# Kernel optimization log

Measured on AMD Instinct MI355X. Metric: run time of the kernel, lower is better.

The kernel has to match this reference:

```python
import jax, jax.numpy as jnp
import numpy as np

DIM_X, DIM_Z, D_MODEL, N_HEADS, BATCH = 512, 256, 256, 8, 32


def sinusoidal_pe(seq_len, d_model):
    # standard sinusoidal table, rows indexed by position
    pos = np.arange(seq_len)[:, None].astype(np.float32)
    div = np.exp(np.arange(0, d_model, 2).astype(np.float32) * (-np.log(10000.0) / d_model))
    pe = np.zeros((seq_len, d_model), dtype=np.float32)
    pe[:, 0::2] = np.sin(pos * div)
    pe[:, 1::2] = np.cos(pos * div)
    return jnp.asarray(pe)


def setup_inputs() -> dict:
    key = jax.random.key(0)
    ks = jax.random.split(key, 5)
    state = jax.random.normal(ks[0], (BATCH, D_MODEL, DIM_X), dtype=jnp.float32)
    obs = jax.random.normal(ks[1], (BATCH, D_MODEL, DIM_Z), dtype=jnp.float32)
    Qp = jax.random.uniform(ks[2], (DIM_X, D_MODEL), dtype=jnp.float32)  # torch.rand init
    Wq = jax.random.normal(ks[3], (D_MODEL, D_MODEL), dtype=jnp.float32) / np.sqrt(D_MODEL)
    Wk = jax.random.normal(ks[4], (D_MODEL, D_MODEL), dtype=jnp.float32) / np.sqrt(D_MODEL)
    bq = jnp.zeros((D_MODEL,), dtype=jnp.float32)
    bk = jnp.zeros((D_MODEL,), dtype=jnp.float32)
    return {"state": state, "obs": obs, "Qp": Qp, "Wq": Wq, "bq": bq, "Wk": Wk, "bk": bk}


def reference(state, obs, Qp, Wq, bq, Wk, bk):
    bs, en, dim_x = state.shape
    dim_z = obs.shape[2]
    d_model = Qp.shape[1]
    h = N_HEADS
    hd = d_model // h
    S = dim_x + dim_z

    # mean-center over the ensemble axis
    A = state - jnp.mean(state, axis=1, keepdims=True)   # [bs, en, dim_x]
    Y = obs - jnp.mean(obs, axis=1, keepdims=True)       # [bs, en, dim_z]
    A = jnp.transpose(A, (2, 0, 1))                      # [dim_x, bs, en]
    Y = jnp.transpose(Y, (2, 0, 1))                      # [dim_z, bs, en]

    # positional encoding: batch_first=True quirk -> PE indexed along axis 1 (the bs axis)
    pe = sinusoidal_pe(bs, d_model)[None, :, :]          # [1, bs, d_model]
    query = Qp[:, None, :] + pe                          # [dim_x, bs, d_model] (broadcast of repeat)
    xy = jnp.concatenate([A, Y], axis=0) + pe            # [S, bs, d_model]

    # multi-head attention weights (V / out-proj do not affect returned quantities)
    q = (query @ Wq.T + bq).reshape(dim_x, bs, h, hd)
    k = (xy @ Wk.T + bk).reshape(S, bs, h, hd)
    scores = jnp.einsum('lbhd,sbhd->bhls', q, k) / np.sqrt(hd)  # [bs, h, dim_x, S]

    # fixed structured mask: eye(dim_x) | bottom-padded eye(dim_z)
    p1 = jnp.eye(dim_x, dtype=bool)
    p2 = jnp.concatenate([jnp.zeros((dim_x - dim_z, dim_z), dtype=bool),
                          jnp.eye(dim_z, dtype=bool)], axis=0)
    allow = jnp.concatenate([p1, p2], axis=1)            # [dim_x, S]
    scores = jnp.where(allow[None, None], scores, -jnp.inf)
    atten = jnp.mean(jax.nn.softmax(scores, axis=-1), axis=1)  # average over heads -> [bs, dim_x, S]

    # weighted merge of the ORIGINAL (uncentered) state/obs
    merge = jnp.concatenate([jnp.transpose(state, (0, 2, 1)),
                             jnp.transpose(obs, (0, 2, 1))], axis=1)  # [bs, S, en]
    new_state = jnp.einsum('bls,bse->ble', atten, merge)              # [bs, dim_x, en]
    new_state = jnp.transpose(new_state, (0, 2, 1))                   # [bs, en, dim_x]
    return new_state, atten
```

## Files before the change

### kernel.cpp

```cpp
#include <hip/hip_runtime.h>
#include <stdint.h>
#include <math.h>


#define WS_P    0
#define WS_QWT  8192
#define WS_PQ   73728
#define WS_U    81920
#define WS_V    606208

typedef float vf4 __attribute__((ext_vector_type(4)));
__device__ __forceinline__ void nt_store4(float* p, float x, float y,
                                          float z, float w) {
  vf4 v; v.x = x; v.y = y; v.z = z; v.w = w;
  __builtin_nontemporal_store(v, (vf4*)p);
}

__global__ void __launch_bounds__(256)
k_qw(const float* __restrict__ Qp, const float* __restrict__ Wq,
     float* __restrict__ ws) {
  int bid = blockIdx.x, t = threadIdx.x;
  if (bid < 64) {
    __shared__ float wq_s[32][132];
    __shared__ float qp_s[32][132];
    int d0 = (bid >> 3) << 5, j0 = (bid & 7) << 5;
    int j = t & 31, dq = t >> 5;
    float acc[4] = {0.f, 0.f, 0.f, 0.f};
    for (int ec = 0; ec < 256; ec += 128) {
      #pragma unroll
      for (int k = 0; k < 4; ++k) {
        int i = (k << 8) + t;
        int r = i >> 5, c4 = i & 31;
        *(float4*)&wq_s[r][c4 << 2] =
            *(const float4*)(Wq + (size_t)(d0 + r) * 256 + ec + (c4 << 2));
        *(float4*)&qp_s[r][c4 << 2] =
            *(const float4*)(Qp + 65536 + (size_t)(j0 + r) * 256 + ec + (c4 << 2));
      }
      __syncthreads();
      #pragma unroll 8
      for (int e4 = 0; e4 < 32; ++e4) {
        float4 q = *(const float4*)&qp_s[j][e4 << 2];
        #pragma unroll
        for (int r = 0; r < 4; ++r) {
          float4 w = *(const float4*)&wq_s[(dq << 2) + r][e4 << 2];
          acc[r] += w.x * q.x + w.y * q.y + w.z * q.z + w.w * q.w;
        }
      }
      __syncthreads();
    }
    #pragma unroll
    for (int r = 0; r < 4; ++r)
      ws[WS_QWT + (size_t)(d0 + (dq << 2) + r) * 256 + j0 + j] = acc[r];
  } else {
    __shared__ float wq_s[32][132];
    __shared__ float pe_s[32][132];
    int d0 = (bid - 64) << 5;
    int b = t & 31, dq = t >> 5;
    float acc[4] = {0.f, 0.f, 0.f, 0.f};
    for (int ec = 0; ec < 256; ec += 128) {
      #pragma unroll
      for (int k = 0; k < 4; ++k) {
        int i = (k << 8) + t;
        int r = i >> 5, c4 = i & 31;
        *(float4*)&wq_s[r][c4 << 2] =
            *(const float4*)(Wq + (size_t)(d0 + r) * 256 + ec + (c4 << 2));
      }
      {
        int b2 = t >> 3, e0 = (t & 7) << 4;
        #pragma unroll
        for (int k = 0; k < 16; ++k) {
          int e = e0 + k;
          int ge = ec + e;
          int k2 = ge & ~1;
          float div = expf((float)k2 * (-9.210340371976184f / 256.f));
          float a = (float)b2 * div;
          pe_s[b2][e] = (ge & 1) ? cosf(a) : sinf(a);
        }
      }
      __syncthreads();
      #pragma unroll 8
      for (int e4 = 0; e4 < 32; ++e4) {
        float4 p = *(const float4*)&pe_s[b][e4 << 2];
        #pragma unroll
        for (int r = 0; r < 4; ++r) {
          float4 w = *(const float4*)&wq_s[(dq << 2) + r][e4 << 2];
          acc[r] += w.x * p.x + w.y * p.y + w.z * p.z + w.w * p.w;
        }
      }
      __syncthreads();
    }
    #pragma unroll
    for (int r = 0; r < 4; ++r)
      ws[WS_PQ + b * 256 + d0 + (dq << 2) + r] = acc[r];
  }
}

__global__ void __launch_bounds__(256)
k_uv(const float* __restrict__ Wk, const float* __restrict__ bq,
     float* __restrict__ ws) {
  int bid = blockIdx.x, t = threadIdx.x;
  if (bid < 256) {
    int h = bid >> 5, e0 = (bid & 31) << 3;
    __shared__ float wk_s[32][9];
    {
      int d = t >> 3, i = t & 7;
      wk_s[d][i] = Wk[(size_t)(h * 32 + d) * 256 + e0 + i];
    }
    __syncthreads();
    float acc[8] = {0.f, 0.f, 0.f, 0.f, 0.f, 0.f, 0.f, 0.f};
    const float* __restrict__ Qw = ws + WS_QWT + t;
    #pragma unroll 4
    for (int d = 0; d < 32; ++d) {
      float q = Qw[((h << 5) + d) << 8];
      #pragma unroll
      for (int i = 0; i < 8; ++i) acc[i] += wk_s[d][i] * q;
    }
    float* Uh = ws + WS_U + (h << 16) + (size_t)e0 * 256;
    #pragma unroll
    for (int i = 0; i < 8; ++i) Uh[(size_t)i * 256 + t] = acc[i];
  } else {
    int idx = bid - 256, b = idx >> 3, h = idx & 7;
    float acc = 0.f;
#pragma unroll 8
    for (int dd = 0; dd < 32; ++dd) {
      int d = h * 32 + dd;
      acc += (ws[WS_PQ + b * 256 + d] + bq[d]) * Wk[(size_t)d * 256 + t];
    }
    ws[WS_V + ((b << 3) + h) * 256 + t] = acc;
  }
}

__global__ void __launch_bounds__(256)
k_delta(const float* __restrict__ state, const float* __restrict__ obs,
        float* __restrict__ ws, float* __restrict__ out) {
  int bid = blockIdx.x, t = threadIdx.x;
  if (bid < 256) {
    int b = bid >> 3, jt = (bid & 7) << 5;
    __shared__ float Xs[256][33];
    __shared__ float Vs[2048];
    __shared__ float pd[8][8][32];
    __shared__ float pw[8][8][32];
    __shared__ float px[8][32];
    __shared__ float pfin[32];
    {
      int es = t >> 3, jq = t & 7;
      const float* sp = state + (size_t)b * 131072 + 256 + jt + (jq << 2);
      const float* op = obs   + (size_t)b * 65536  + jt + (jq << 2);
      #pragma unroll
      for (int k = 0; k < 8; ++k) {
        int e = es + (k << 5);
        float4 s4 = *(const float4*)(sp + (size_t)e * 512);
        float4 o4 = *(const float4*)(op + (size_t)e * 256);
        float* xr = &Xs[e][jq << 2];
        xr[0] = s4.x - o4.x; xr[1] = s4.y - o4.y;
        xr[2] = s4.z - o4.z; xr[3] = s4.w - o4.w;
      }
      for (int i = t; i < 2048; i += 256) Vs[i] = ws[WS_V + (b << 11) + i];
    }
    __syncthreads();
    int j = t & 31, eg = t >> 5, e0 = eg << 5;
    {
      float ax = 0.f;
      #pragma unroll
      for (int ei = 0; ei < 32; ++ei) ax += Xs[e0 + ei][j];
      px[eg][j] = ax;
    }
    const float* __restrict__ Ub = ws + WS_U + jt + j;
    #pragma unroll
    for (int h = 0; h < 8; ++h) {
      float dacc = 0.f, wacc = 0.f;
      const float* __restrict__ Uh = Ub + (h << 16) + (e0 << 8);
      const float* __restrict__ Vh = Vs + (h << 8) + e0;
      #pragma unroll 16
      for (int ei = 0; ei < 32; ++ei) {
        float w = Uh[ei << 8] + Vh[ei];
        dacc += Xs[e0 + ei][j] * w;
        wacc += w;
      }
      pd[eg][h][j] = dacc;
      pw[eg][h][j] = wacc;
    }
    __syncthreads();
    int h2 = t >> 5, j2 = t & 31;
    float D = 0.f, W = 0.f, X = 0.f;
    #pragma unroll
    for (int g = 0; g < 8; ++g) {
      D += pd[g][h2][j2];
      W += pw[g][h2][j2];
      X += px[g][j2];
    }
    float delta = D - X * (1.f / 256.f) * W;
    float sig = 1.f / (1.f + __expf(-delta * 0.17677669529663687f));
    __syncthreads();
    px[h2][j2] = sig;
    __syncthreads();
    if (t < 32) {
      float acc = 0.f;
      #pragma unroll
      for (int h = 0; h < 8; ++h) acc += px[h][t];
      float p = acc * 0.125f;
      pfin[t] = p;
      int l = 256 + jt + t;
      size_t rb = 4194304 + (size_t)((b << 9) + l) * 768;
      int c1 = l >> 2, pos = l & 3;
      float v1[4] = {0.f, 0.f, 0.f, 0.f}; v1[pos] = p;
      nt_store4(out + rb + (c1 << 2), v1[0], v1[1], v1[2], v1[3]);
      float v2[4] = {0.f, 0.f, 0.f, 0.f}; v2[pos] = 1.f - p;
      nt_store4(out + rb + ((c1 + 64) << 2), v2[0], v2[1], v2[2], v2[3]);
    }
    __syncthreads();
    {
      int eb = t >> 3, j0 = (t & 7) << 2;
      const float* op2 = obs + (size_t)b * 65536 + jt + j0;
      float p0 = pfin[j0], p1 = pfin[j0 + 1], p2 = pfin[j0 + 2], p3 = pfin[j0 + 3];
      float* orow = out + (size_t)b * 131072 + 256 + jt + j0;
      #pragma unroll
      for (int k = 0; k < 8; ++k) {
        int e = eb + (k << 5);
        float4 o4 = *(const float4*)(op2 + (size_t)e * 256);
        const float* xr = &Xs[e][j0];
        nt_store4(orow + (size_t)e * 512,
                  o4.x + p0 * xr[0], o4.y + p1 * xr[1],
                  o4.z + p2 * xr[2], o4.w + p3 * xr[3]);
      }
    }
  } else if (bid < 2304) {
    int row = ((bid - 256) << 2) | (t >> 6);
    int c = t & 63;
    float4 sv = ((const float4*)(state + (size_t)row * 512))[c];
    nt_store4(out + (size_t)row * 512 + (c << 2), sv.x, sv.y, sv.z, sv.w);
  } else {
    int g4 = (bid - 2304) * 256 + t;
    int r = g4 / 192, c = g4 - r * 192;
    int b = r >> 9, l = r & 511;
    int s0 = c << 2;
    if (l < 256) {
      float v[4] = {0.f, 0.f, 0.f, 0.f};
      if (l >= s0 && l < s0 + 4) v[l - s0] = 1.0f;
      nt_store4(out + 4194304 + ((size_t)g4 << 2), v[0], v[1], v[2], v[3]);
    } else {
      int c1 = l >> 2;
      if (c != c1 && c != c1 + 64)
        nt_store4(out + 4194304 + ((size_t)g4 << 2), 0.f, 0.f, 0.f, 0.f);
    }
  }
}

extern "C" void kernel_launch(void* const* d_in, const int* in_sizes, int n_in,
                              void* d_out, int out_size, void* d_ws, size_t ws_size,
                              hipStream_t stream) {
  const float *state = nullptr, *obs = nullptr, *Qp = nullptr;
  const float *Wq = nullptr, *Wk = nullptr, *bq = nullptr, *bk = nullptr;
  for (int i = 0; i < n_in; ++i) {
    int s = in_sizes[i];
    const float* p = (const float*)d_in[i];
    if      (s == 4194304) state = p;
    else if (s == 2097152) obs = p;
    else if (s == 131072)  Qp = p;
    else if (s == 65536)   { if (!Wq) Wq = p; else Wk = p; }
    else if (s == 256)     { if (!bq) bq = p; else bk = p; }
  }
  (void)bk;
  float* out = (float*)d_out;
  float* ws  = (float*)d_ws;

  k_qw   <<<72,    256, 0, stream>>>(Qp, Wq, ws);
  k_uv   <<<512,   256, 0, stream>>>(Wk, bq, ws);
  k_delta<<<14592, 256, 0, stream>>>(state, obs, ws, out);
}
```

Before: 118.8 us.

## Fuse query-weight and U/V precompute kernels into a single launch

New measurement: 130.9 us. +10.2%, slower.

```diff
diff --git a/kernel.cpp b/kernel.cpp
--- a/kernel.cpp
+++ b/kernel.cpp
@@ -3,9 +3,6 @@
 #include <math.h>
 
 
-#define WS_P    0
-#define WS_QWT  8192
-#define WS_PQ   73728
 #define WS_U    81920
 #define WS_V    606208
 
@@ -17,13 +14,17 @@
 }
 
 __global__ void __launch_bounds__(256)
-k_qw(const float* __restrict__ Qp, const float* __restrict__ Wq,
-     float* __restrict__ ws) {
+k_uvw(const float* __restrict__ Qp, const float* __restrict__ Wq,
+      const float* __restrict__ Wk, const float* __restrict__ bq,
+      float* __restrict__ ws) {
+  __shared__ float A[9504];
   int bid = blockIdx.x, t = threadIdx.x;
   if (bid < 64) {
-    __shared__ float wq_s[32][132];
-    __shared__ float qp_s[32][132];
-    int d0 = (bid >> 3) << 5, j0 = (bid & 7) << 5;
+    int h = bid >> 3, j0 = (bid & 7) << 5;
+    int d0 = h << 5;
+    float* wq_s  = A;
+    float* qp_s  = A + 4224;
+    float* qwt_s = A + 8448;
     int j = t & 31, dq = t >> 5;
     float acc[4] = {0.f, 0.f, 0.f, 0.f};
     for (int ec = 0; ec < 256; ec += 128) {
@@ -31,18 +32,18 @@
       for (int k = 0; k < 4; ++k) {
         int i = (k << 8) + t;
         int r = i >> 5, c4 = i & 31;
-        *(float4*)&wq_s[r][c4 << 2] =
+        *(float4*)&wq_s[r * 132 + (c4 << 2)] =
             *(const float4*)(Wq + (size_t)(d0 + r) * 256 + ec + (c4 << 2));
-        *(float4*)&qp_s[r][c4 << 2] =
+        *(float4*)&qp_s[r * 132 + (c4 << 2)] =
             *(const float4*)(Qp + 65536 + (size_t)(j0 + r) * 256 + ec + (c4 << 2));
       }
       __syncthreads();
       #pragma unroll 8
       for (int e4 = 0; e4 < 32; ++e4) {
-        float4 q = *(const float4*)&qp_s[j][e4 << 2];
+        float4 q = *(const float4*)&qp_s[j * 132 + (e4 << 2)];
         #pragma unroll
         for (int r = 0; r < 4; ++r) {
-          float4 w = *(const float4*)&wq_s[(dq << 2) + r][e4 << 2];
+          float4 w = *(const float4*)&wq_s[((dq << 2) + r) * 132 + (e4 << 2)];
           acc[r] += w.x * q.x + w.y * q.y + w.z * q.z + w.w * q.w;
         }
       }
@@ -50,82 +51,68 @@
     }
     #pragma unroll
     for (int r = 0; r < 4; ++r)
-      ws[WS_QWT + (size_t)(d0 + (dq << 2) + r) * 256 + j0 + j] = acc[r];
-  } else {
-    __shared__ float wq_s[32][132];
-    __shared__ float pe_s[32][132];
-    int d0 = (bid - 64) << 5;
-    int b = t & 31, dq = t >> 5;
-    float acc[4] = {0.f, 0.f, 0.f, 0.f};
+      qwt_s[((dq << 2) + r) * 33 + j] = acc[r];
+    __syncthreads();
+    float* wk_s = A;
     for (int ec = 0; ec < 256; ec += 128) {
       #pragma unroll
       for (int k = 0; k < 4; ++k) {
         int i = (k << 8) + t;
         int r = i >> 5, c4 = i & 31;
-        *(float4*)&wq_s[r][c4 << 2] =
-            *(const float4*)(Wq + (size_t)(d0 + r) * 256 + ec + (c4 << 2));
-      }
-      {
-        int b2 = t >> 3, e0 = (t & 7) << 4;
+        *(float4*)&wk_s[r * 132 + (c4 << 2)] =
+            *(const float4*)(Wk + (size_t)(d0 + r) * 256 + ec + (c4 << 2));
+      }
+      __syncthreads();
+      int es8 = t >> 5;
+      float* Uh = ws + WS_U + (h << 16) + j0 + j;
+      #pragma unroll
+      for (int k = 0; k < 16; ++k) {
+        int el = es8 + (k << 3);
+        float u = 0.f;
         #pragma unroll
-        for (int k = 0; k < 16; ++k) {
-          int e = e0 + k;
-          int ge = ec + e;
-          int k2 = ge & ~1;
-          float div = expf((float)k2 * (-9.210340371976184f / 256.f));
-          float a = (float)b2 * div;
-          pe_s[b2][e] = (ge & 1) ? cosf(a) : sinf(a);
-        }
-      }
-      __syncthreads();
-      #pragma unroll 8
-      for (int e4 = 0; e4 < 32; ++e4) {
-        float4 p = *(const float4*)&pe_s[b][e4 << 2];
-        #pragma unroll
-        for (int r = 0; r < 4; ++r) {
-          float4 w = *(const float4*)&wq_s[(dq << 2) + r][e4 << 2];
-          acc[r] += w.x * p.x + w.y * p.y + w.z * p.z + w.w * p.w;
-        }
-      }
-      __syncthreads();
-    }
-    #pragma unroll
-    for (int r = 0; r < 4; ++r)
-      ws[WS_PQ + b * 256 + d0 + (dq << 2) + r] = acc[r];
-  }
-}
-
-__global__ void __launch_bounds__(256)
-k_uv(const float* __restrict__ Wk, const float* __restrict__ bq,
-     float* __restrict__ ws) {
-  int bid = blockIdx.x, t = threadIdx.x;
-  if (bid < 256) {
-    int h = bid >> 5, e0 = (bid & 31) << 3;
-    __shared__ float wk_s[32][9];
-    {
-      int d = t >> 3, i = t & 7;
-      wk_s[d][i] = Wk[(size_t)(h * 32 + d) * 256 + e0 + i];
-    }
-    __syncthreads();
-    float acc[8] = {0.f, 0.f, 0.f, 0.f, 0.f, 0.f, 0.f, 0.f};
-    const float* __restrict__ Qw = ws + WS_QWT + t;
-    #pragma unroll 4
-    for (int d = 0; d < 32; ++d) {
-      float q = Qw[((h << 5) + d) << 8];
-      #pragma unroll
-      for (int i = 0; i < 8; ++i) acc[i] += wk_s[d][i] * q;
-    }
-    float* Uh = ws + WS_U + (h << 16) + (size_t)e0 * 256;
-    #pragma unroll
-    for (int i = 0; i < 8; ++i) Uh[(size_t)i * 256 + t] = acc[i];
+        for (int d = 0; d < 32; ++d)
+          u += qwt_s[d * 33 + j] * wk_s[d * 132 + el];
+        Uh[(size_t)(ec + el) << 8] = u;
+      }
+      __syncthreads();
+    }
   } else {
-    int idx = bid - 256, b = idx >> 3, h = idx & 7;
+    int idx = bid - 64, b = idx >> 3, h = idx & 7;
+    float* pe_s = A;
+    float* psum = A + 256;
+    float* pq_s = A + 544;
+    {
+      int k2 = t & ~1;
+      float div = expf((float)k2 * (-9.210340371976184f / 256.f));
+      float a = (float)b * div;
+      pe_s[t] = (t & 1) ? cosf(a) : sinf(a);
+    }
+    __syncthreads();
+    {
+      int d8 = t >> 3, c8 = t & 7;
+      const float* wrow = Wq + (size_t)((h << 5) + d8) * 256 + (c8 << 5);
+      const float* prow = pe_s + (c8 << 5);
+      float part = 0.f;
+      #pragma unroll
+      for (int i = 0; i < 8; ++i) {
+        float4 w4 = *(const float4*)(wrow + (i << 2));
+        float4 p4 = *(const float4*)(prow + (i << 2));
+        part += w4.x * p4.x + w4.y * p4.y + w4.z * p4.z + w4.w * p4.w;
+      }
+      psum[d8 * 9 + c8] = part;
+    }
+    __syncthreads();
+    if (t < 32) {
+      float s = bq[(h << 5) + t];
+      #pragma unroll
+      for (int c8 = 0; c8 < 8; ++c8) s += psum[t * 9 + c8];
+      pq_s[t] = s;
+    }
+    __syncthreads();
     float acc = 0.f;
-#pragma unroll 8
-    for (int dd = 0; dd < 32; ++dd) {
-      int d = h * 32 + dd;
-      acc += (ws[WS_PQ + b * 256 + d] + bq[d]) * Wk[(size_t)d * 256 + t];
-    }
+    #pragma unroll 8
+    for (int dd = 0; dd < 32; ++dd)
+      acc += pq_s[dd] * Wk[(size_t)((h << 5) + dd) * 256 + t];
     ws[WS_V + ((b << 3) + h) * 256 + t] = acc;
   }
 }
@@ -264,7 +251,6 @@
   float* out = (float*)d_out;
   float* ws  = (float*)d_ws;
 
-  k_qw   <<<72,    256, 0, stream>>>(Qp, Wq, ws);
-  k_uv   <<<512,   256, 0, stream>>>(Wk, bq, ws);
+  k_uvw  <<<320,   256, 0, stream>>>(Qp, Wq, Wk, bq, ws);
   k_delta<<<14592, 256, 0, stream>>>(state, obs, ws, out);
 }
```
